# Kernel tuning notes

Hardware: AMD Instinct MI355X
Metric: run time of the kernel (lower is better)

## Reference

```python
import jax, jax.numpy as jnp
import numpy as np
import math

B, S, D, H, L, DFF, NB = 32, 512, 768, 8, 6, 3072, 12
TBINS = 100
CLIP = 512
HD = D // H


def _alibi_slopes(n):
    start = 2.0 ** (-(2.0 ** (-(math.log2(n) - 3))))
    return np.array([start ** (i + 1) for i in range(n)], dtype=np.float32)


def setup_inputs():
    key = jax.random.key(0)
    ks = jax.random.split(key, 32)
    s = 0.02
    inp = {}
    inp['sensor_ids'] = jax.random.randint(ks[0], (B, S), 0, 2000)
    inp['state_ids'] = jax.random.randint(ks[1], (B, S), 0, 16)
    inp['room_ids'] = jax.random.randint(ks[2], (B, S), 0, 64)
    inp['coordinates'] = jax.random.uniform(ks[3], (B, S, 2), dtype=jnp.float32)
    inp['time_deltas'] = jax.random.uniform(ks[4], (B, S), dtype=jnp.float32) * 3600.0
    inp['mask'] = jnp.ones((B, S), dtype=bool)
    inp['emb_sensor'] = jax.random.normal(ks[5], (2000, D)) * s
    inp['emb_state'] = jax.random.normal(ks[6], (16, D)) * s
    inp['emb_room'] = jax.random.normal(ks[7], (64, D)) * s
    inp['fourier_W'] = jax.random.normal(ks[8], (4 * NB, D)) * s
    inp['fourier_b'] = jnp.zeros((D,))
    inp['time_emb'] = jax.random.normal(ks[9], (TBINS, D)) * s
    inp['cls_token'] = jax.random.normal(ks[10], (1, 1, D))
    inp['pos_emb'] = jax.random.normal(ks[11], (1, S + 1, D)) * s
    inp['ln1_g'] = jnp.ones((L, D)); inp['ln1_b'] = jnp.zeros((L, D))
    inp['Wq'] = jax.random.normal(ks[12], (L, D, D)) * s; inp['bq'] = jnp.zeros((L, D))
    inp['Wk'] = jax.random.normal(ks[13], (L, D, D)) * s; inp['bk'] = jnp.zeros((L, D))
    inp['Wv'] = jax.random.normal(ks[14], (L, D, D)) * s; inp['bv'] = jnp.zeros((L, D))
    inp['Wo'] = jax.random.normal(ks[15], (L, D, D)) * s; inp['bo'] = jnp.zeros((L, D))
    inp['ln2_g'] = jnp.ones((L, D)); inp['ln2_b'] = jnp.zeros((L, D))
    inp['W1'] = jax.random.normal(ks[16], (L, D, DFF)) * s; inp['b1'] = jnp.zeros((L, DFF))
    inp['W2'] = jax.random.normal(ks[17], (L, DFF, D)) * s; inp['b2'] = jnp.zeros((L, D))
    inp['lnf_g'] = jnp.ones((D,)); inp['lnf_b'] = jnp.zeros((D,))
    inp['pool_W'] = jax.random.normal(ks[18], (D, D)) * s; inp['pool_b'] = jnp.zeros((D,))
    inp['clip_W'] = jax.random.normal(ks[19], (D, CLIP)) * s
    return inp


def _ln(x, g, b):
    m = jnp.mean(x, -1, keepdims=True)
    v = jnp.mean((x - m) ** 2, -1, keepdims=True)
    return (x - m) * jax.lax.rsqrt(v + 1e-5) * g + b


def _encode(sensor_ids, state_ids, room_ids, coordinates, time_deltas, mask,
            emb_sensor, emb_state, emb_room, fourier_W, fourier_b, time_emb,
            cls_token, pos_emb, ln1_g, ln1_b, Wq, bq, Wk, bk, Wv, bv, Wo, bo,
            ln2_g, ln2_b, W1, b1, W2, b2, lnf_g, lnf_b, pool_W, pool_b, clip_W):
    b_, s_ = coordinates.shape[:2]
    # multi-field embedding fusion
    tok = emb_sensor[sensor_ids] + emb_state[state_ids] + emb_room[room_ids]
    # Fourier features: [B,S,2,1] * [NB] -> [B,S,2,NB], cat sin/cos -> [B,S,4*NB]
    freqs = 2.0 ** jnp.arange(NB, dtype=coordinates.dtype)
    ang = coordinates[..., None] * freqs * math.pi
    ff = jnp.concatenate([jnp.sin(ang), jnp.cos(ang)], -1).reshape(b_, s_, 4 * NB)
    tok = tok + (ff @ fourier_W + fourier_b)
    # log-bucketed time deltas
    td = jnp.clip(time_deltas, 1e-6, None)
    idx = (jnp.log(td + 1.0) / math.log(3600.0 + 1.0) * (TBINS - 1)).astype(jnp.int32)
    idx = jnp.clip(idx, 0, TBINS - 1)
    tok = tok + time_emb[idx]
    x = jnp.concatenate([jnp.broadcast_to(cls_token, (b_, 1, D)), tok], axis=1)
    x = x + pos_emb[:, :s_ + 1]
    extmask = jnp.concatenate([jnp.ones((b_, 1), dtype=bool), mask], axis=1)
    # ALiBi bias [H, S+1, S+1]
    slopes = jnp.asarray(_alibi_slopes(H))
    pos = jnp.arange(s_ + 1)
    dist = jnp.abs(pos[None, :] - pos[:, None]).astype(x.dtype)
    bias = -dist[None, :, :] * slopes[:, None, None]
    neg_inf = jnp.asarray(-jnp.inf, dtype=x.dtype)

    def layer(x, p):
        l1g, l1b, wq, bq_, wk, bk_, wv, bv_, wo, bo_, l2g, l2b, w1, b1_, w2, b2_ = p
        h = _ln(x, l1g, l1b)
        q = (h @ wq + bq_).reshape(b_, s_ + 1, H, HD)
        k = (h @ wk + bk_).reshape(b_, s_ + 1, H, HD)
        v = (h @ wv + bv_).reshape(b_, s_ + 1, H, HD)
        sc = jnp.einsum('bqhd,bkhd->bhqk', q, k) / math.sqrt(HD) + bias
        sc = jnp.where(extmask[:, None, None, :], sc, neg_inf)
        a = jax.nn.softmax(sc, axis=-1)
        o = jnp.einsum('bhqk,bkhd->bqhd', a, v).reshape(b_, s_ + 1, D)
        x = x + (o @ wo + bo_)
        h2 = _ln(x, l2g, l2b)
        x = x + (jax.nn.gelu(h2 @ w1 + b1_, approximate=False) @ w2 + b2_)
        return x, None

    x, _ = jax.lax.scan(layer, x, (ln1_g, ln1_b, Wq, bq, Wk, bk, Wv, bv, Wo, bo,
                                   ln2_g, ln2_b, W1, b1, W2, b2))
    x = _ln(x, lnf_g, lnf_b)
    cls = x[:, 0]
    mf = mask.astype(x.dtype)
    mean = (x[:, 1:] * mf[..., None]).sum(1) / jnp.clip(mf.sum(1, keepdims=True), 1.0, None)
    pooled = (0.5 * cls + 0.5 * mean) @ pool_W + pool_b
    clip = pooled @ clip_W
    return clip / jnp.linalg.norm(clip, axis=-1, keepdims=True)


def reference(sensor_ids, state_ids, room_ids, coordinates, time_deltas, mask,
              emb_sensor, emb_state, emb_room, fourier_W, fourier_b, time_emb,
              cls_token, pos_emb, ln1_g, ln1_b, Wq, bq, Wk, bk, Wv, bv, Wo, bo,
              ln2_g, ln2_b, W1, b1, W2, b2, lnf_g, lnf_b, pool_W, pool_b, clip_W):
    return _encode(sensor_ids, state_ids, room_ids, coordinates, time_deltas, mask,
                   emb_sensor, emb_state, emb_room, fourier_W, fourier_b, time_emb,
                   cls_token, pos_emb, ln1_g, ln1_b, Wq, bq, Wk, bk, Wv, bv, Wo, bo,
                   ln2_g, ln2_b, W1, b1, W2, b2, lnf_g, lnf_b, pool_W, pool_b, clip_W)
```

## Files before the change

### kernel.cpp

```cpp
#include <hip/hip_runtime.h>
#include <hip/hip_bf16.h>
#include <cmath>

#define B_   32
#define S_   512
#define SP1  513
#define D_   768
#define H_   8
#define HD_  96
#define L_   6
#define DFF_ 3072
#define NTOK (B_*SP1)
#define VTP  520

typedef short short8 __attribute__((ext_vector_type(8)));
typedef float f32x4  __attribute__((ext_vector_type(4)));

__device__ __forceinline__ short f2bf(float f){
  unsigned u = __float_as_uint(f);
  u += 0x7fffu + ((u >> 16) & 1u);
  return (short)(u >> 16);
}

__device__ __forceinline__ int xcd_swz(int orig, int nwg){
  int q = nwg >> 3, r = nwg & 7;
  int x = orig & 7, idx = orig >> 3;
  return (x < r ? x*(q+1) : r*(q+1) + (x-r)*q) + idx;
}

__device__ __forceinline__ void gload_lds16(const short* g, short* l){
  __builtin_amdgcn_global_load_lds((const __attribute__((address_space(1))) void*)g,
                                   (__attribute__((address_space(3))) void*)l, 16, 0, 0);
}

__device__ __forceinline__ float block_sum256(float v, float* tmp){
  #pragma unroll
  for (int o = 32; o; o >>= 1) v += __shfl_xor(v, o, 64);
  int t = threadIdx.x;
  if ((t & 63) == 0) tmp[t >> 6] = v;
  __syncthreads();
  float r = tmp[0] + tmp[1] + tmp[2] + tmp[3];
  __syncthreads();
  return r;
}

__device__ __forceinline__ void block_sum2(float& a, float& b, float* tmp){
  #pragma unroll
  for (int o = 32; o; o >>= 1){ a += __shfl_xor(a, o, 64); b += __shfl_xor(b, o, 64); }
  int t = threadIdx.x;
  if ((t & 63) == 0){ tmp[(t >> 6)*2] = a; tmp[(t >> 6)*2 + 1] = b; }
  __syncthreads();
  a = tmp[0] + tmp[2] + tmp[4] + tmp[6];
  b = tmp[1] + tmp[3] + tmp[5] + tmp[7];
  __syncthreads();
}

__global__ __launch_bounds__(256) void embed_kernel(
    const int* __restrict__ sensor_ids, const int* __restrict__ state_ids,
    const int* __restrict__ room_ids, const float* __restrict__ coords,
    const float* __restrict__ tdelt,
    const float* __restrict__ emb_sensor, const float* __restrict__ emb_state,
    const float* __restrict__ emb_room, const float* __restrict__ fourier_W,
    const float* __restrict__ fourier_b, const float* __restrict__ time_emb,
    const float* __restrict__ cls_tok, const float* __restrict__ pos_emb,
    float* __restrict__ x){
  __shared__ float ffs[16][48];
  __shared__ int meta[16][4];
  int t = threadIdx.x;
  int tok0 = blockIdx.x * 16;
  if (t < 16){
    int tk = tok0 + t;
    int b = tk / SP1, p = tk % SP1;
    int sid=0, stid=0, rid=0, tidx=0;
    if (p){
      int s = p - 1;
      sid  = sensor_ids[b*S_+s]; stid = state_ids[b*S_+s]; rid = room_ids[b*S_+s];
      float td = fmaxf(tdelt[b*S_+s], 1e-6f);
      float fi = logf(td + 1.0f) / logf(3601.0f) * 99.0f;
      int ix = (int)fi;
      tidx = ix < 0 ? 0 : (ix > 99 ? 99 : ix);
    }
    meta[t][0]=sid; meta[t][1]=stid; meta[t][2]=rid; meta[t][3]=tidx;
  }
  for (int i = t; i < 16*24; i += 256){
    int tl = i / 24, r = i % 24;
    int c = r / 12, f = r % 12;
    int tk = tok0 + tl;
    int b = tk / SP1, p = tk % SP1;
    float sv = 0.f, cv = 0.f;
    if (p){
      float ang = coords[((size_t)b*S_ + (p-1))*2 + c] * exp2f((float)f) * 3.14159265358979323846f;
      sv = sinf(ang); cv = cosf(ang);
    }
    ffs[tl][c*24 + f]      = sv;
    ffs[tl][c*24 + 12 + f] = cv;
  }
  __syncthreads();
  for (int dc = 0; dc < 3; dc++){
    int d = dc*256 + t;
    float acc[16];
    #pragma unroll
    for (int tl=0; tl<16; tl++) acc[tl] = 0.f;
    for (int f = 0; f < 48; f++){
      float wv = fourier_W[f*D_ + d];
      #pragma unroll
      for (int tl=0; tl<16; tl++) acc[tl] += ffs[tl][f] * wv;
    }
    float fb = fourier_b[d];
    for (int tl = 0; tl < 16; tl++){
      int tk = tok0 + tl;
      int b = tk / SP1, p = tk % SP1;
      float v;
      if (p == 0) v = cls_tok[d] + pos_emb[d];
      else v = emb_sensor[(size_t)meta[tl][0]*D_ + d] + emb_state[(size_t)meta[tl][1]*D_ + d]
             + emb_room[(size_t)meta[tl][2]*D_ + d] + time_emb[(size_t)meta[tl][3]*D_ + d]
             + fb + acc[tl] + pos_emb[(size_t)p*D_ + d];
      x[(size_t)tk*D_ + d] = v;
    }
  }
}

template<typename OUT>
__global__ __launch_bounds__(256) void ln_kernel(const float* __restrict__ x,
    const float* __restrict__ g, const float* __restrict__ bb, OUT* __restrict__ out){
  __shared__ float tmp[8];
  int row = blockIdx.x, t = threadIdx.x;
  const float* xr = x + (size_t)row*D_;
  float v0 = xr[t], v1 = xr[t+256], v2 = xr[t+512];
  float s1 = v0+v1+v2, s2 = v0*v0 + v1*v1 + v2*v2;
  block_sum2(s1, s2, tmp);
  float mean = s1 * (1.f/768.f);
  float var  = fmaxf(s2 * (1.f/768.f) - mean*mean, 0.f);
  float rstd = rsqrtf(var + 1e-5f);
  OUT* orow = out + (size_t)row*D_;
  float r0 = (v0-mean)*rstd*g[t]     + bb[t];
  float r1 = (v1-mean)*rstd*g[t+256] + bb[t+256];
  float r2 = (v2-mean)*rstd*g[t+512] + bb[t+512];
  if constexpr (sizeof(OUT) == 2){
    orow[t] = f2bf(r0); orow[t+256] = f2bf(r1); orow[t+512] = f2bf(r2);
  } else {
    orow[t] = r0; orow[t+256] = r1; orow[t+512] = r2;
  }
}

__global__ __launch_bounds__(256) void transpose6_kernel(
    const float* __restrict__ Wq, const float* __restrict__ Wk,
    const float* __restrict__ Wv, const float* __restrict__ Wo,
    const float* __restrict__ W1, const float* __restrict__ W2,
    short* __restrict__ wqkvT, short* __restrict__ woT,
    short* __restrict__ w1T, short* __restrict__ w2T){
  __shared__ float tile[32][33];
  int bid = blockIdx.x;
  const float* W; short* WT; int K, Nn, tb;
  if (bid < 576)       { W=Wq; WT=wqkvT;                    K=768;  Nn=768;  tb=bid; }
  else if (bid < 1152) { W=Wk; WT=wqkvT+(size_t)768*768;    K=768;  Nn=768;  tb=bid-576; }
  else if (bid < 1728) { W=Wv; WT=wqkvT+(size_t)1536*768;   K=768;  Nn=768;  tb=bid-1152; }
  else if (bid < 2304) { W=Wo; WT=woT;                      K=768;  Nn=768;  tb=bid-1728; }
  else if (bid < 4608) { W=W1; WT=w1T;                      K=768;  Nn=3072; tb=bid-2304; }
  else                 { W=W2; WT=w2T;                      K=3072; Nn=768;  tb=bid-4608; }
  int nt = Nn >> 5;
  int bx = tb % nt, by = tb / nt;
  int tx = threadIdx.x & 31, ty = threadIdx.x >> 5;
  #pragma unroll
  for (int i = 0; i < 4; i++)
    tile[ty + i*8][tx] = W[(size_t)(by*32 + ty + i*8)*Nn + bx*32 + tx];
  __syncthreads();
  #pragma unroll
  for (int i = 0; i < 4; i++)
    WT[(size_t)(bx*32 + ty + i*8)*K + by*32 + tx] = f2bf(tile[tx][ty + i*8]);
}

__global__ __launch_bounds__(256) void concat_bias_kernel(const float* __restrict__ bq,
    const float* __restrict__ bk, const float* __restrict__ bv, float* __restrict__ bc){
  int i = blockIdx.x*256 + threadIdx.x;
  if (i >= 6*2304) return;
  int l = i / 2304, j = i % 2304;
  float v;
  if (j < 768)       v = bq[l*768 + j];
  else if (j < 1536) v = bk[l*768 + j - 768];
  else               v = bv[l*768 + j - 1536];
  bc[i] = v;
}

template<int EPI>
__global__ __launch_bounds__(256) void gemm_bt(const short* __restrict__ A,
    const short* __restrict__ BT, const float* __restrict__ bias,
    void* __restrict__ Cp, short* __restrict__ VtG,
    int M, int K, int ldc, int Ntiles, int nwg){
  __shared__ __align__(16) union SMem {
    struct { short A[2][128][32]; short B[2][128][32]; } k;
    short eh[4][16][72];
    float ef[4][16][72];
  } sm;
  int wg = xcd_swz(blockIdx.x, nwg);
  int bm = wg / Ntiles, bn = wg % Ntiles;
  int t = threadIdx.x, lane = t & 63, w = t >> 6;
  int wm = (w >> 1)*64, wn = (w & 1)*64;
  int lr = lane & 15, lg = lane >> 4;
  int sr = lane >> 2;
  int sg = ((lane & 3) ^ ((lane >> 3) & 3)) * 8;
  int KT = K >> 5;

  auto stage = [&](short (*Ad)[32], short (*Bd)[32], int kt){
    int k0 = kt*32;
    #pragma unroll
    for (int i = 0; i < 2; i++){
      int r = w*32 + i*16 + sr;
      int arow = bm*128 + r; if (arow >= M) arow = M-1;
      gload_lds16(A + (size_t)arow*K + k0 + sg, &Ad[w*32 + i*16][0]);
      int brow = bn*128 + r;
      gload_lds16(BT + (size_t)brow*K + k0 + sg, &Bd[w*32 + i*16][0]);
    }
  };

  f32x4 acc[4][4] = {};
  stage(sm.k.A[0], sm.k.B[0], 0);
  stage(sm.k.A[1], sm.k.B[1], 1);
  int rg = (lg ^ ((lr >> 1) & 3)) * 8;

  for (int kt = 0; kt < KT; kt += 2){
    asm volatile("s_waitcnt vmcnt(4)" ::: "memory");
    __builtin_amdgcn_sched_barrier(0);
    __builtin_amdgcn_s_barrier();
    {
      short8 a[4], b[4];
      #pragma unroll
      for (int m = 0; m < 4; m++) a[m] = *reinterpret_cast<const short8*>(&sm.k.A[0][wm + m*16 + lr][rg]);
      #pragma unroll
      for (int n = 0; n < 4; n++) b[n] = *reinterpret_cast<const short8*>(&sm.k.B[0][wn + n*16 + lr][rg]);
      asm volatile("s_waitcnt lgkmcnt(0)" ::: "memory");
      __builtin_amdgcn_sched_barrier(0);
      __builtin_amdgcn_s_setprio(1);
      #pragma unroll
      for (int m = 0; m < 4; m++)
        #pragma unroll
        for (int n = 0; n < 4; n++)
          acc[m][n] = __builtin_amdgcn_mfma_f32_16x16x32_bf16(a[m], b[n], acc[m][n], 0, 0, 0);
      __builtin_amdgcn_s_setprio(0);
    }
    __builtin_amdgcn_s_barrier();
    { int kn = kt + 2; if (kn > KT-1) kn = KT-1; stage(sm.k.A[0], sm.k.B[0], kn); }

    asm volatile("s_waitcnt vmcnt(4)" ::: "memory");
    __builtin_amdgcn_sched_barrier(0);
    __builtin_amdgcn_s_barrier();
    {
      short8 a[4], b[4];
      #pragma unroll
      for (int m = 0; m < 4; m++) a[m] = *reinterpret_cast<const short8*>(&sm.k.A[1][wm + m*16 + lr][rg]);
      #pragma unroll
      for (int n = 0; n < 4; n++) b[n] = *reinterpret_cast<const short8*>(&sm.k.B[1][wn + n*16 + lr][rg]);
      asm volatile("s_waitcnt lgkmcnt(0)" ::: "memory");
      __builtin_amdgcn_sched_barrier(0);
      __builtin_amdgcn_s_setprio(1);
      #pragma unroll
      for (int m = 0; m < 4; m++)
        #pragma unroll
        for (int n = 0; n < 4; n++)
          acc[m][n] = __builtin_amdgcn_mfma_f32_16x16x32_bf16(a[m], b[n], acc[m][n], 0, 0, 0);
      __builtin_amdgcn_s_setprio(0);
    }
    __builtin_amdgcn_s_barrier();
    { int kn = kt + 3; if (kn > KT-1) kn = KT-1; stage(sm.k.A[1], sm.k.B[1], kn); }
  }

  asm volatile("s_waitcnt vmcnt(0)" ::: "memory");
  __syncthreads();

  int cbaseW = bn*128 + wn;
  int growW  = bm*128 + wm;

  if constexpr (EPI == 2){
    #pragma unroll
    for (int m = 0; m < 4; m++){
      asm volatile("s_waitcnt lgkmcnt(0)" ::: "memory");
      #pragma unroll
      for (int n = 0; n < 4; n++)
        #pragma unroll
        for (int j = 0; j < 4; j++)
          sm.ef[w][lg*4 + j][n*16 + lr] = acc[m][n][j] + bias[cbaseW + n*16 + lr];
      asm volatile("s_waitcnt lgkmcnt(0)" ::: "memory");
      #pragma unroll
      for (int cc = 0; cc < 4; cc++){
        int c = lane + cc*64;
        int row = c >> 4, seg = c & 15;
        int grow = growW + m*16 + row;
        if (grow < M){
          float* gp = (float*)Cp + (size_t)grow*ldc + cbaseW + seg*4;
          f32x4 add = *reinterpret_cast<const f32x4*>(&sm.ef[w][row][seg*4]);
          f32x4 old = *reinterpret_cast<const f32x4*>(gp);
          *reinterpret_cast<f32x4*>(gp) = old + add;
        }
      }
    }
  } else {
    bool vtg_block = (EPI == 0) && (cbaseW >= 1536);
    if (!vtg_block){
      #pragma unroll
      for (int m = 0; m < 4; m++){
        asm volatile("s_waitcnt lgkmcnt(0)" ::: "memory");
        #pragma unroll
        for (int n = 0; n < 4; n++)
          #pragma unroll
          for (int j = 0; j < 4; j++){
            float v = acc[m][n][j] + bias[cbaseW + n*16 + lr];
            if constexpr (EPI == 1) v = 0.5f*v*(1.0f + erff(v*0.70710678118654752f));
            sm.eh[w][lg*4 + j][n*16 + lr] = f2bf(v);
          }
        asm volatile("s_waitcnt lgkmcnt(0)" ::: "memory");
        #pragma unroll
        for (int cc = 0; cc < 2; cc++){
          int c = lane + cc*64;
          int row = c >> 3, seg = c & 7;
          int grow = growW + m*16 + row;
          if (grow < M)
            *reinterpret_cast<short8*>((short*)Cp + (size_t)grow*ldc + cbaseW + seg*8) =
                *reinterpret_cast<const short8*>(&sm.eh[w][row][seg*8]);
        }
      }
    } else {
      #pragma unroll
      for (int m = 0; m < 4; m++){
        #pragma unroll
        for (int n = 0; n < 4; n++){
          int col = cbaseW + n*16 + lr;
          #pragma unroll
          for (int j = 0; j < 4; j++){
            int row = growW + lg*4 + m*16 + j;
            if (row < M){
              float v = acc[m][n][j] + bias[col];
              int bb = row / SP1, kp = row - bb*SP1;
              int c  = col - 1536;
              int hh = c / 96, d = c - hh*96;
              VtG[((size_t)(bb*8 + hh)*96 + d)*VTP + kp] = f2bf(v);
            }
          }
        }
      }
    }
  }
}

__global__ __launch_bounds__(256) void attn_kernel(const short* __restrict__ qkv,
                                                   const short* __restrict__ VtG,
                                                   short* __restrict__ o){
  __shared__ __align__(16) short Plds[4][16][72];
  __shared__ __align__(16) short Vt[96][72];
  int wg = xcd_swz(blockIdx.x, 2304);
  int qt = wg % 9; int hh = (wg / 9) & 7; int b = wg / 72;
  int t = threadIdx.x, lane = t & 63, w = t >> 6;
  int lr = lane & 15, lg = lane >> 4;
  int q0 = qt*64 + w*16;
  const int RS = 1536;
  const short* base = qkv + (size_t)b*SP1*RS + hh*HD_;
  const short* kb = base + D_;
  const short* vg = VtG + (size_t)(b*8 + hh)*96*VTP;
  int qrow = q0 + lr; if (qrow > 512) qrow = 512;
  short8 qf[3];
  #pragma unroll
  for (int ks = 0; ks < 3; ks++)
    qf[ks] = *reinterpret_cast<const short8*>(base + (size_t)qrow*RS + ks*32 + lg*8);
  float m[4]    = {-1e30f, -1e30f, -1e30f, -1e30f};
  float lsum[4] = {0.f, 0.f, 0.f, 0.f};
  f32x4 oacc[6] = {};
  float slope = exp2f(-(float)(hh + 1));
  const float scale = 0.10206207261596577f;
  for (int t0 = 0; t0 < SP1; t0 += 64){
    __syncthreads();
    #pragma unroll
    for (int ii = 0; ii < 3; ii++){
      int i = t + ii*256;
      int r = i >> 3, c = (i & 7)*8;
      *reinterpret_cast<short8*>(&Vt[r][c]) =
          *reinterpret_cast<const short8*>(vg + (size_t)r*VTP + t0 + c);
    }
    f32x4 s[4] = {};
    __builtin_amdgcn_s_setprio(1);
    #pragma unroll
    for (int st = 0; st < 4; st++){
      int tr = t0 + st*16 + lr; if (tr > 512) tr = 512;
      #pragma unroll
      for (int ks = 0; ks < 3; ks++){
        short8 kf = *reinterpret_cast<const short8*>(kb + (size_t)tr*RS + ks*32 + lg*8);
        s[st] = __builtin_amdgcn_mfma_f32_16x16x32_bf16(qf[ks], kf, s[st], 0, 0, 0);
      }
    }
    __builtin_amdgcn_s_setprio(0);
    #pragma unroll
    for (int j = 0; j < 4; j++){
      int qr = q0 + lg*4 + j;
      float v[4]; float mx = -1e30f;
      #pragma unroll
      for (int st = 0; st < 4; st++){
        int tc = t0 + st*16 + lr;
        float sv = s[st][j]*scale - slope*fabsf((float)(qr - tc));
        if (tc > 512) sv = -1e30f;
        v[st] = sv; mx = fmaxf(mx, sv);
      }
      mx = fmaxf(mx, __shfl_xor(mx, 1, 64));
      mx = fmaxf(mx, __shfl_xor(mx, 2, 64));
      mx = fmaxf(mx, __shfl_xor(mx, 4, 64));
      mx = fmaxf(mx, __shfl_xor(mx, 8, 64));
      float mn = fmaxf(m[j], mx);
      float corr = __expf(m[j] - mn);
      float rs = 0.f;
      #pragma unroll
      for (int st = 0; st < 4; st++){ v[st] = __expf(v[st] - mn); rs += v[st]; }
      rs += __shfl_xor(rs, 1, 64); rs += __shfl_xor(rs, 2, 64);
      rs += __shfl_xor(rs, 4, 64); rs += __shfl_xor(rs, 8, 64);
      lsum[j] = lsum[j]*corr + rs;
      m[j] = mn;
      #pragma unroll
      for (int n = 0; n < 6; n++) oacc[n][j] *= corr;
      #pragma unroll
      for (int st = 0; st < 4; st++) Plds[w][lg*4 + j][st*16 + lr] = f2bf(v[st]);
    }
    __syncthreads();
    short8 pf0 = *reinterpret_cast<const short8*>(&Plds[w][lr][lg*8]);
    short8 pf1 = *reinterpret_cast<const short8*>(&Plds[w][lr][32 + lg*8]);
    __builtin_amdgcn_s_setprio(1);
    #pragma unroll
    for (int n = 0; n < 6; n++){
      short8 vf0 = *reinterpret_cast<const short8*>(&Vt[n*16 + lr][lg*8]);
      short8 vf1 = *reinterpret_cast<const short8*>(&Vt[n*16 + lr][32 + lg*8]);
      oacc[n] = __builtin_amdgcn_mfma_f32_16x16x32_bf16(pf0, vf0, oacc[n], 0, 0, 0);
      oacc[n] = __builtin_amdgcn_mfma_f32_16x16x32_bf16(pf1, vf1, oacc[n], 0, 0, 0);
    }
    __builtin_amdgcn_s_setprio(0);
  }
  #pragma unroll
  for (int j = 0; j < 4; j++){
    int qr = q0 + lg*4 + j;
    if (qr <= 512){
      float inv = 1.0f / lsum[j];
      #pragma unroll
      for (int n = 0; n < 6; n++)
        o[((size_t)b*SP1 + qr)*D_ + hh*HD_ + n*16 + lr] = f2bf(oacc[n][j]*inv);
    }
  }
}

__global__ __launch_bounds__(256) void pool1_kernel(const float* __restrict__ lnfb,
                                                    float* __restrict__ part){
  int bid = blockIdx.x; int b = bid >> 3, c = bid & 7;
  int t = threadIdx.x;
  for (int d = t; d < D_; d += 256){
    const float* pb = lnfb + (size_t)b*SP1*D_ + d;
    float s = 0.f;
    for (int i = 1 + c*64; i <= (c+1)*64; i++) s += pb[(size_t)i*D_];
    part[(size_t)bid*D_ + d] = s;
  }
}

__global__ __launch_bounds__(256) void pool2_kernel(const float* __restrict__ lnfb,
    const float* __restrict__ part, float* __restrict__ pooled_in){
  int b = blockIdx.x, t = threadIdx.x;
  for (int d = t; d < D_; d += 256){
    float s = 0.f;
    #pragma unroll
    for (int c = 0; c < 8; c++) s += part[(size_t)(b*8+c)*D_ + d];
    pooled_in[b*D_ + d] = 0.5f*lnfb[(size_t)b*SP1*D_ + d] + 0.5f*(s*(1.0f/512.0f));
  }
}

__global__ __launch_bounds__(256) void matvec_kernel(const float* __restrict__ in,
    const float* __restrict__ W, const float* __restrict__ bias,
    float* __restrict__ out, int K, int Nn){
  __shared__ float inr[768];
  int nb = Nn >> 8;
  int b = blockIdx.x / nb, jc = blockIdx.x % nb;
  int t = threadIdx.x;
  for (int d = t; d < K; d += 256) inr[d] = in[(size_t)b*K + d];
  __syncthreads();
  int j = jc*256 + t;
  float acc = bias ? bias[j] : 0.0f;
  for (int d = 0; d < K; d++) acc += inr[d]*W[(size_t)d*Nn + j];
  out[(size_t)b*Nn + j] = acc;
}

__global__ __launch_bounds__(256) void norm_kernel(const float* __restrict__ c,
                                                   float* __restrict__ out){
  __shared__ float tmp[4];
  int b = blockIdx.x, t = threadIdx.x;
  float v0 = c[b*512 + t], v1 = c[b*512 + 256 + t];
  float s = block_sum256(v0*v0 + v1*v1, tmp);
  float inv = 1.0f / sqrtf(s);
  out[b*512 + t]       = v0*inv;
  out[b*512 + 256 + t] = v1*inv;
}

extern "C" void kernel_launch(void* const* d_in, const int* in_sizes, int n_in,
                              void* d_out, int out_size, void* d_ws, size_t ws_size,
                              hipStream_t stream){
  const int*   sensor_ids = (const int*)d_in[0];
  const int*   state_ids  = (const int*)d_in[1];
  const int*   room_ids   = (const int*)d_in[2];
  const float* coords     = (const float*)d_in[3];
  const float* tdelt      = (const float*)d_in[4];
  const float* emb_sensor = (const float*)d_in[6];
  const float* emb_state  = (const float*)d_in[7];
  const float* emb_room   = (const float*)d_in[8];
  const float* fourier_W  = (const float*)d_in[9];
  const float* fourier_b  = (const float*)d_in[10];
  const float* time_emb   = (const float*)d_in[11];
  const float* cls_tok    = (const float*)d_in[12];
  const float* pos_emb    = (const float*)d_in[13];
  const float* ln1_g = (const float*)d_in[14];
  const float* ln1_b = (const float*)d_in[15];
  const float* Wq = (const float*)d_in[16];
  const float* bq = (const float*)d_in[17];
  const float* Wk = (const float*)d_in[18];
  const float* bk = (const float*)d_in[19];
  const float* Wv = (const float*)d_in[20];
  const float* bv = (const float*)d_in[21];
  const float* Wo = (const float*)d_in[22];
  const float* bo = (const float*)d_in[23];
  const float* ln2_g = (const float*)d_in[24];
  const float* ln2_b = (const float*)d_in[25];
  const float* W1 = (const float*)d_in[26];
  const float* b1 = (const float*)d_in[27];
  const float* W2 = (const float*)d_in[28];
  const float* b2 = (const float*)d_in[29];
  const float* lnf_g = (const float*)d_in[30];
  const float* lnf_b = (const float*)d_in[31];
  const float* pool_W = (const float*)d_in[32];
  const float* pool_b = (const float*)d_in[33];
  const float* clip_W = (const float*)d_in[34];

  const size_t QKV_SH = (size_t)NTOK*1536;
  const size_t VTG_SH = (size_t)256*96*VTP;
  const size_t OB_SH  = (size_t)NTOK*D_;
  size_t big_bytes = (QKV_SH + VTG_SH + OB_SH)*2;

  char* p = (char*)d_ws;
  float* x       = (float*)p; p += (size_t)NTOK*D_*4;
  short* h       = (short*)p; p += (size_t)NTOK*D_*2;
  short* big     = (short*)p; p += big_bytes;
  short* wT      = (short*)p; p += (size_t)7077888*2;
  float* biascat = (float*)p; p += (size_t)6*2304*4;
  float* part      = (float*)p; p += (size_t)256*768*4;
  float* pooled_in = (float*)p; p += (size_t)32*768*4;
  float* pooled    = (float*)p; p += (size_t)32*768*4;
  float* clipv     = (float*)p; p += (size_t)32*512*4;

  short* qkvb  = big;
  short* vtg   = big + QKV_SH;
  short* ob    = vtg + VTG_SH;
  short* wqkvT = wT;
  short* woT   = wqkvT + (size_t)2304*768;
  short* w1T   = woT   + (size_t)768*768;
  short* w2T   = w1T   + (size_t)3072*768;
  float* lnfb  = (float*)big;

  embed_kernel<<<NTOK/16, 256, 0, stream>>>(sensor_ids, state_ids, room_ids, coords, tdelt,
      emb_sensor, emb_state, emb_room, fourier_W, fourier_b, time_emb, cls_tok, pos_emb, x);
  concat_bias_kernel<<<54, 256, 0, stream>>>(bq, bk, bv, biascat);

  for (int l = 0; l < 6; l++){
    transpose6_kernel<<<6912, 256, 0, stream>>>(
        Wq + (size_t)l*589824, Wk + (size_t)l*589824, Wv + (size_t)l*589824,
        Wo + (size_t)l*589824, W1 + (size_t)l*2359296, W2 + (size_t)l*2359296,
        wqkvT, woT, w1T, w2T);

    ln_kernel<short><<<NTOK, 256, 0, stream>>>(x, ln1_g + l*768, ln1_b + l*768, h);
    gemm_bt<0><<<129*18, 256, 0, stream>>>(h, wqkvT, biascat + l*2304, qkvb, vtg,
                                           NTOK, 768, 1536, 18, 129*18);
    attn_kernel<<<2304, 256, 0, stream>>>(qkvb, vtg, ob);
    gemm_bt<2><<<129*6, 256, 0, stream>>>(ob, woT, bo + l*768, x, nullptr,
                                          NTOK, 768, 768, 6, 129*6);
    ln_kernel<short><<<NTOK, 256, 0, stream>>>(x, ln2_g + l*768, ln2_b + l*768, h);
    gemm_bt<1><<<129*24, 256, 0, stream>>>(h, w1T, b1 + l*3072, big, nullptr,
                                           NTOK, 768, 3072, 24, 129*24);
    gemm_bt<2><<<129*6, 256, 0, stream>>>(big, w2T, b2 + l*768, x, nullptr,
                                          NTOK, 3072, 768, 6, 129*6);
  }

  ln_kernel<float><<<NTOK, 256, 0, stream>>>(x, lnf_g, lnf_b, lnfb);
  pool1_kernel<<<256, 256, 0, stream>>>(lnfb, part);
  pool2_kernel<<<32, 256, 0, stream>>>(lnfb, part, pooled_in);
  matvec_kernel<<<96, 256, 0, stream>>>(pooled_in, pool_W, pool_b, pooled, 768, 768);
  matvec_kernel<<<64, 256, 0, stream>>>(pooled, clip_W, nullptr, clipv, 768, 512);
  norm_kernel<<<32, 256, 0, stream>>>(clipv, (float*)d_out);
}
```

Before: 3.680 ms.

## Prefetch V tiles into registers, skip tail work, and lazily rescale softmax

The attention kernel now loads the next V tile from global memory into registers while the current tile is processed, so load latency overlaps compute. The final partial key tile (only one valid key) skips three of the four QK MFMA groups and half of the PV MFMAs. The online softmax skips the max reduction and accumulator rescaling unless some lane's row max exceeds the running max by more than a threshold, which removes shuffles and multiplies on most tiles. This adds register pressure and a wave-level branch, and the lazy rescale relies on exponent headroom to stay numerically safe.

```diff
diff --git a/kernel.cpp b/kernel.cpp
--- a/kernel.cpp
+++ b/kernel.cpp
@@ -365,19 +365,35 @@
   f32x4 oacc[6] = {};
   float slope = exp2f(-(float)(hh + 1));
   const float scale = 0.10206207261596577f;
+
+  short8 vv[3];
+  #pragma unroll
+  for (int ii = 0; ii < 3; ii++){
+    int i = t + ii*256;
+    vv[ii] = *reinterpret_cast<const short8*>(vg + (size_t)(i >> 3)*VTP + (i & 7)*8);
+  }
+
   for (int t0 = 0; t0 < SP1; t0 += 64){
+    bool tail = (t0 == 512);
     __syncthreads();
     #pragma unroll
     for (int ii = 0; ii < 3; ii++){
       int i = t + ii*256;
-      int r = i >> 3, c = (i & 7)*8;
-      *reinterpret_cast<short8*>(&Vt[r][c]) =
-          *reinterpret_cast<const short8*>(vg + (size_t)r*VTP + t0 + c);
+      *reinterpret_cast<short8*>(&Vt[i >> 3][(i & 7)*8]) = vv[ii];
+    }
+    {
+      int tp = t0 + 64; if (tp > 512) tp = 512;
+      #pragma unroll
+      for (int ii = 0; ii < 3; ii++){
+        int i = t + ii*256;
+        vv[ii] = *reinterpret_cast<const short8*>(vg + (size_t)(i >> 3)*VTP + tp + (i & 7)*8);
+      }
     }
     f32x4 s[4] = {};
     __builtin_amdgcn_s_setprio(1);
     #pragma unroll
     for (int st = 0; st < 4; st++){
+      if (st && tail) break;
       int tr = t0 + st*16 + lr; if (tr > 512) tr = 512;
       #pragma unroll
       for (int ks = 0; ks < 3; ks++){
@@ -386,45 +402,77 @@
       }
     }
     __builtin_amdgcn_s_setprio(0);
+    float v[4][4]; float mxl[4]; bool need = false;
     #pragma unroll
     for (int j = 0; j < 4; j++){
       int qr = q0 + lg*4 + j;
-      float v[4]; float mx = -1e30f;
+      float mx = -3e38f;
       #pragma unroll
       for (int st = 0; st < 4; st++){
         int tc = t0 + st*16 + lr;
-        float sv = s[st][j]*scale - slope*fabsf((float)(qr - tc));
+        float sv = (tail && st) ? -1e30f
+                 : s[st][j]*scale - slope*fabsf((float)(qr - tc));
         if (tc > 512) sv = -1e30f;
-        v[st] = sv; mx = fmaxf(mx, sv);
-      }
-      mx = fmaxf(mx, __shfl_xor(mx, 1, 64));
-      mx = fmaxf(mx, __shfl_xor(mx, 2, 64));
-      mx = fmaxf(mx, __shfl_xor(mx, 4, 64));
-      mx = fmaxf(mx, __shfl_xor(mx, 8, 64));
-      float mn = fmaxf(m[j], mx);
-      float corr = __expf(m[j] - mn);
-      float rs = 0.f;
-      #pragma unroll
-      for (int st = 0; st < 4; st++){ v[st] = __expf(v[st] - mn); rs += v[st]; }
-      rs += __shfl_xor(rs, 1, 64); rs += __shfl_xor(rs, 2, 64);
-      rs += __shfl_xor(rs, 4, 64); rs += __shfl_xor(rs, 8, 64);
-      lsum[j] = lsum[j]*corr + rs;
-      m[j] = mn;
-      #pragma unroll
-      for (int n = 0; n < 6; n++) oacc[n][j] *= corr;
-      #pragma unroll
-      for (int st = 0; st < 4; st++) Plds[w][lg*4 + j][st*16 + lr] = f2bf(v[st]);
+        v[j][st] = sv; mx = fmaxf(mx, sv);
+      }
+      mxl[j] = mx;
+      need |= (mx > m[j] + 8.f);
+    }
+    if (__any(need)){
+      #pragma unroll
+      for (int j = 0; j < 4; j++){
+        float mx = mxl[j];
+        mx = fmaxf(mx, __shfl_xor(mx, 1, 64));
+        mx = fmaxf(mx, __shfl_xor(mx, 2, 64));
+        mx = fmaxf(mx, __shfl_xor(mx, 4, 64));
+        mx = fmaxf(mx, __shfl_xor(mx, 8, 64));
+        float mn = fmaxf(m[j], mx);
+        float corr = __expf(m[j] - mn);
+        float rs = 0.f;
+        #pragma unroll
+        for (int st = 0; st < 4; st++){
+          float p = __expf(v[j][st] - mn); rs += p;
+          Plds[w][lg*4 + j][st*16 + lr] = f2bf(p);
+        }
+        rs += __shfl_xor(rs, 1, 64); rs += __shfl_xor(rs, 2, 64);
+        rs += __shfl_xor(rs, 4, 64); rs += __shfl_xor(rs, 8, 64);
+        lsum[j] = lsum[j]*corr + rs;
+        m[j] = mn;
+        #pragma unroll
+        for (int n = 0; n < 6; n++) oacc[n][j] *= corr;
+      }
+    } else {
+      #pragma unroll
+      for (int j = 0; j < 4; j++){
+        float rs = 0.f;
+        #pragma unroll
+        for (int st = 0; st < 4; st++){
+          float p = __expf(v[j][st] - m[j]); rs += p;
+          Plds[w][lg*4 + j][st*16 + lr] = f2bf(p);
+        }
+        rs += __shfl_xor(rs, 1, 64); rs += __shfl_xor(rs, 2, 64);
+        rs += __shfl_xor(rs, 4, 64); rs += __shfl_xor(rs, 8, 64);
+        lsum[j] += rs;
+      }
     }
     __syncthreads();
     short8 pf0 = *reinterpret_cast<const short8*>(&Plds[w][lr][lg*8]);
-    short8 pf1 = *reinterpret_cast<const short8*>(&Plds[w][lr][32 + lg*8]);
     __builtin_amdgcn_s_setprio(1);
-    #pragma unroll
-    for (int n = 0; n < 6; n++){
-      short8 vf0 = *reinterpret_cast<const short8*>(&Vt[n*16 + lr][lg*8]);
-      short8 vf1 = *reinterpret_cast<const short8*>(&Vt[n*16 + lr][32 + lg*8]);
-      oacc[n] = __builtin_amdgcn_mfma_f32_16x16x32_bf16(pf0, vf0, oacc[n], 0, 0, 0);
-      oacc[n] = __builtin_amdgcn_mfma_f32_16x16x32_bf16(pf1, vf1, oacc[n], 0, 0, 0);
+    if (!tail){
+      short8 pf1 = *reinterpret_cast<const short8*>(&Plds[w][lr][32 + lg*8]);
+      #pragma unroll
+      for (int n = 0; n < 6; n++){
+        short8 vf0 = *reinterpret_cast<const short8*>(&Vt[n*16 + lr][lg*8]);
+        short8 vf1 = *reinterpret_cast<const short8*>(&Vt[n*16 + lr][32 + lg*8]);
+        oacc[n] = __builtin_amdgcn_mfma_f32_16x16x32_bf16(pf0, vf0, oacc[n], 0, 0, 0);
+        oacc[n] = __builtin_amdgcn_mfma_f32_16x16x32_bf16(pf1, vf1, oacc[n], 0, 0, 0);
+      }
+    } else {
+      #pragma unroll
+      for (int n = 0; n < 6; n++){
+        short8 vf0 = *reinterpret_cast<const short8*>(&Vt[n*16 + lr][lg*8]);
+        oacc[n] = __builtin_amdgcn_mfma_f32_16x16x32_bf16(pf0, vf0, oacc[n], 0, 0, 0);
+      }
     }
     __builtin_amdgcn_s_setprio(0);
   }
```

Measured after the change: 3.696 ms. Within noise of the previous version (+0.4%).
